# Optimization experiments

Measured on AMD Instinct MI355X. Metric: run time of the kernel, lower is better.

## Reference

```python
import jax, jax.numpy as jnp
import numpy as np

TAU = 0.001
TEMPERATURE = 0.1


def setup_inputs() -> dict:
    key = jax.random.key(0)
    k1, k2 = jax.random.split(key)
    B, H, N, L = 2, 8, 256, 64
    X = jax.random.normal(k1, (B, H, N, L), dtype=jnp.float32)
    Y = jax.random.normal(k2, (B, H, N, L), dtype=jnp.float32)
    return {"X": X, "Y": Y}


def _softsort_p2(scores):
    # scores: [B,H,N,L] -> s: [B,H,L,N]
    s = jnp.transpose(scores, (0, 1, 3, 2))
    srt = -jnp.sort(-s, axis=-1)  # descending sort along N
    # pairwise squared diff: rows = sorted values, cols = original values -> [B,H,L,N,N]
    pd = -((s[..., None, :] - srt[..., :, None]) ** 2) / TAU
    return jax.nn.softmax(pd, axis=-1)


def reference(X, Y):
    # Soft permutation matrices: [B,H,L,N,N]
    Pu = _softsort_p2(X)
    Pv = _softsort_p2(Y)
    # Gamma = Pu^T @ Pv  (contract over sorted-row index i)
    Gamma = jnp.einsum('bhlij,bhlik->bhljk', Pu, Pv)
    # cdist(X, Y, p=2) over last dim L -> [B,H,N,N]
    x2 = jnp.sum(X * X, axis=-1)            # [B,H,N]
    y2 = jnp.sum(Y * Y, axis=-1)            # [B,H,N]
    xy = jnp.einsum('bhnl,bhml->bhnm', X, Y)
    cost = jnp.sqrt(jnp.maximum(x2[..., :, None] + y2[..., None, :] - 2.0 * xy, 1e-12))
    # swds[b,h,l] = sum_{j,k} cost[b,h,j,k] * Gamma[b,h,l,j,k]
    swds = jnp.einsum('bhjk,bhljk->bhl', cost, Gamma)
    # exp(-T*(swds - min)) / sum == softmax(-T * swds) over L
    weights = jax.nn.softmax(-TEMPERATURE * swds, axis=-1)  # [B,H,L]
    # weighted sum over L -> [B,H,N,N]
    return jnp.einsum('bhljk,bhl->bhjk', Gamma, weights)
```

## Files before the change

### kernel.cpp

```cpp
#include <hip/hip_runtime.h>
#include <math.h>

#define INV_TAU 1000.0f
#define TEMP    0.1f
#define CEXP    -1442.6950408889634f


typedef __attribute__((ext_vector_type(8))) _Float16 half8;
typedef __attribute__((ext_vector_type(8))) short short8;
typedef __attribute__((ext_vector_type(4))) float f32x4;
typedef __attribute__((ext_vector_type(2))) unsigned int u32x2;

__device__ __forceinline__ float fexp2(float x) { return __builtin_amdgcn_exp2f(x); }

__device__ __forceinline__ half8 ldsh8(const unsigned short* p) {
  return __builtin_bit_cast(half8, *(const short8*)p);
}

__device__ __forceinline__ unsigned bf16r(float f) {
  unsigned u = __float_as_uint(f);
  return (u + 0x7FFFu + ((u >> 16) & 1u)) >> 16;
}

__device__ __forceinline__ int tswz(int row, int g) {
  return row * 32 + (((g + (row >> 1)) & 3) << 3);
}

__global__ __launch_bounds__(256) void prep_kernel(const float* __restrict__ X,
                                                   const float* __restrict__ Y,
                                                   float* __restrict__ cost,
                                                   float* __restrict__ srtu, float* __restrict__ lziu,
                                                   float* __restrict__ srtv, float* __restrict__ lziv) {
  __shared__ __align__(16) float smem[256];
  const int tid = threadIdx.x;
  if (blockIdx.x < 1024) {
    const int jq = blockIdx.x & 63, bh = blockIdx.x >> 6;
    const int j0 = jq * 4;
    smem[tid] = X[((size_t)bh*256 + j0 + (tid >> 6))*64 + (tid & 63)];
    __syncthreads();
    const float4* yp = (const float4*)(Y + ((size_t)bh*256 + tid)*64);
    float dot[4] = {0.f,0.f,0.f,0.f}, x2[4] = {0.f,0.f,0.f,0.f}, y2 = 0.f;
#pragma unroll
    for (int t = 0; t < 16; ++t) {
      float4 yv = yp[t];
      y2 += yv.x*yv.x + yv.y*yv.y + yv.z*yv.z + yv.w*yv.w;
#pragma unroll
      for (int r = 0; r < 4; ++r) {
        float4 xv = ((const float4*)(smem + r*64))[t];
        dot[r] += xv.x*yv.x + xv.y*yv.y + xv.z*yv.z + xv.w*yv.w;
        x2[r]  += xv.x*xv.x + xv.y*xv.y + xv.z*xv.z + xv.w*xv.w;
      }
    }
#pragma unroll
    for (int r = 0; r < 4; ++r) {
      float c = x2[r] + y2 - 2.f*dot[r];
      cost[((size_t)bh*256 + j0 + r)*256 + tid] = sqrtf(fmaxf(c, 1e-12f));
    }
  } else {
    const int idx = blockIdx.x - 1024;
    const int l = idx & 63, bh = (idx >> 6) & 15, uv = idx >> 10;
    const float* S = uv ? Y : X;
    float* so = uv ? srtv : srtu;
    float* zo = uv ? lziv : lziu;
    float v = S[((size_t)bh*256 + tid)*64 + l];
#pragma unroll
    for (int k = 2; k <= 256; k <<= 1) {
#pragma unroll
      for (int j = k >> 1; j > 0; j >>= 1) {
        float o;
        if (j >= 64) {
          smem[tid] = v; __syncthreads();
          o = smem[tid ^ j]; __syncthreads();
        } else {
          o = __shfl_xor(v, j, 64);
        }
        const bool up    = ((tid & k) == 0);
        const bool lower = ((tid & j) == 0);
        float mn = fminf(v, o), mx = fmaxf(v, o);
        v = (up == lower) ? mn : mx;
      }
    }
    smem[tid] = v; __syncthreads();
    const int jc = 255 - tid;
    const float sv = smem[jc];
    const int lo = jc > 48 ? jc - 48 : 0;
    const int hi = jc < 207 ? jc + 48 : 255;
    float z = 0.f;
    for (int jj = lo; jj <= hi; ++jj) { float d = smem[jj] - sv; z += fexp2(d*d*CEXP); }
    const int base = (bh*64 + l)*256 + tid;
    so[base] = sv; zo[base] = -__log2f(z);
  }
}

__device__ __forceinline__ void stage_slab(int t, int ib, float uval, float vval,
                                           const float* __restrict__ srtU, const float* __restrict__ lziU,
                                           const float* __restrict__ srtV, const float* __restrict__ lziV,
                                           unsigned short* __restrict__ EU,
                                           unsigned short* __restrict__ EV) {
  const int r  = t & 127;
  const int gp = (t >> 7) << 1;
  const int i0 = ib + (gp << 3);
#pragma unroll
  for (int gg = 0; gg < 2; ++gg) {
    float e[8];
#pragma unroll
    for (int ii = 0; ii < 8; ++ii) {
      float d = uval - srtU[i0 + gg*8 + ii];
      e[ii] = fexp2(fmaf(d*d, CEXP, lziU[i0 + gg*8 + ii]));
    }
    uint4 w;
    w.x = __builtin_bit_cast(unsigned, __builtin_amdgcn_cvt_pkrtz(e[0], e[1]));
    w.y = __builtin_bit_cast(unsigned, __builtin_amdgcn_cvt_pkrtz(e[2], e[3]));
    w.z = __builtin_bit_cast(unsigned, __builtin_amdgcn_cvt_pkrtz(e[4], e[5]));
    w.w = __builtin_bit_cast(unsigned, __builtin_amdgcn_cvt_pkrtz(e[6], e[7]));
    *(uint4*)&EU[tswz(r, gp + gg)] = w;
  }
#pragma unroll
  for (int gg = 0; gg < 2; ++gg) {
    float e[8];
#pragma unroll
    for (int ii = 0; ii < 8; ++ii) {
      float d = vval - srtV[i0 + gg*8 + ii];
      e[ii] = fexp2(fmaf(d*d, CEXP, lziV[i0 + gg*8 + ii]));
    }
    uint4 w;
    w.x = __builtin_bit_cast(unsigned, __builtin_amdgcn_cvt_pkrtz(e[0], e[1]));
    w.y = __builtin_bit_cast(unsigned, __builtin_amdgcn_cvt_pkrtz(e[2], e[3]));
    w.z = __builtin_bit_cast(unsigned, __builtin_amdgcn_cvt_pkrtz(e[4], e[5]));
    w.w = __builtin_bit_cast(unsigned, __builtin_amdgcn_cvt_pkrtz(e[6], e[7]));
    *(uint4*)&EV[tswz(r, gp + gg)] = w;
  }
}

__global__ __launch_bounds__(256, 4) void pass1_kernel(
    const float* __restrict__ X, const float* __restrict__ Y,
    const float* __restrict__ cost,
    const float* __restrict__ srtu, const float* __restrict__ lziu,
    const float* __restrict__ srtv, const float* __restrict__ lziv,
    float* __restrict__ parts, u32x2* __restrict__ gamma) {
  const int tile = blockIdx.x, l = blockIdx.y, bh = blockIdx.z;
  const int j0 = (tile >> 1) * 128, k0 = (tile & 1) * 128;
  const int tid = threadIdx.x, wave = tid >> 6, lane = tid & 63;
  const int wj = (wave & 1) * 64, wk = (wave >> 1) * 64;
  const int m = lane & 15, q = lane >> 4;
  const int inner = m*32 + (((q + (m >> 1)) & 3) << 3);

  __shared__ float srtU[256], lziU[256], srtV[256], lziV[256];
  __shared__ __align__(16) unsigned short EU0[128*32], EU1[128*32];
  __shared__ __align__(16) unsigned short EV0[128*32], EV1[128*32];
  __shared__ float red[4];

  const int lb = (bh*64 + l)*256;
  const int r  = tid & 127;
  const float uval = X[((size_t)bh*256 + j0 + r)*64 + l];
  const float vval = Y[((size_t)bh*256 + k0 + r)*64 + l];
  srtU[tid] = srtu[lb + tid]; lziU[tid] = lziu[lb + tid];
  srtV[tid] = srtv[lb + tid]; lziV[tid] = lziv[lb + tid];

  f32x4 acc[16];
#pragma unroll
  for (int t = 0; t < 16; ++t) acc[t] = (f32x4){0.f, 0.f, 0.f, 0.f};

  __syncthreads();
  stage_slab(tid, 0, uval, vval, srtU, lziU, srtV, lziV, EU0, EV0);
  __syncthreads();
#pragma unroll 1
  for (int s = 0; s < 8; ++s) {
    const unsigned short* EUc = (s & 1) ? EU1 : EU0;
    const unsigned short* EVc = (s & 1) ? EV1 : EV0;
    unsigned short* EUn = (s & 1) ? EU0 : EU1;
    unsigned short* EVn = (s & 1) ? EV0 : EV1;
    half8 A[4], B[4];
#pragma unroll
    for (int mt = 0; mt < 4; ++mt) A[mt] = ldsh8(&EUc[(wj + mt*16)*32 + inner]);
#pragma unroll
    for (int nt = 0; nt < 4; ++nt) B[nt] = ldsh8(&EVc[(wk + nt*16)*32 + inner]);
    if (s < 7)
      stage_slab(tid, (s+1)*32, uval, vval, srtU, lziU, srtV, lziV, EUn, EVn);
#pragma unroll
    for (int mt = 0; mt < 4; ++mt)
#pragma unroll
      for (int nt = 0; nt < 4; ++nt)
        acc[mt*4+nt] = __builtin_amdgcn_mfma_f32_16x16x32_f16(A[mt], B[nt], acc[mt*4+nt], 0, 0, 0);
    __syncthreads();
  }

  const float* cb = cost + (size_t)bh * 65536;
  const int gbase = ((bh*4 + tile)*4 + wave) * 16;
  float part = 0.f;
#pragma unroll
  for (int mt = 0; mt < 4; ++mt) {
#pragma unroll
    for (int nt = 0; nt < 4; ++nt) {
      const int col  = k0 + wk + nt*16 + m;
      const int rowb = j0 + wj + mt*16 + q*4;
      f32x4 a = acc[mt*4 + nt];
      part += a.x*cb[(size_t)(rowb+0)*256 + col] + a.y*cb[(size_t)(rowb+1)*256 + col]
            + a.z*cb[(size_t)(rowb+2)*256 + col] + a.w*cb[(size_t)(rowb+3)*256 + col];
      u32x2 pk;
      pk.x = bf16r(a.x) | (bf16r(a.y) << 16);
      pk.y = bf16r(a.z) | (bf16r(a.w) << 16);
      __builtin_nontemporal_store(pk, &gamma[((size_t)(gbase + mt*4 + nt)*64 + l)*64 + lane]);
    }
  }
#pragma unroll
  for (int o = 32; o > 0; o >>= 1) part += __shfl_down(part, o, 64);
  if (lane == 0) red[wave] = part;
  __syncthreads();
  if (tid == 0) parts[(size_t)tile*1024 + bh*64 + l] = red[0] + red[1] + red[2] + red[3];
}

__global__ __launch_bounds__(256) void wsum_kernel(const u32x2* __restrict__ g,
                                                   const float* __restrict__ parts,
                                                   float* __restrict__ out) {
  const int wv = threadIdx.x >> 6, lane = threadIdx.x & 63;
  const int bh = blockIdx.x >> 6;
  __shared__ float w[64];
  if (wv == 0) {
    float s = parts[bh*64 + lane] + parts[1024 + bh*64 + lane]
            + parts[2048 + bh*64 + lane] + parts[3072 + bh*64 + lane];
    float v = -TEMP * s * 1.4426950408889634f;
    float mx = v;
#pragma unroll
    for (int o = 32; o > 0; o >>= 1) mx = fmaxf(mx, __shfl_xor(mx, o, 64));
    float e = fexp2(v - mx);
    float ssum = e;
#pragma unroll
    for (int o = 32; o > 0; o >>= 1) ssum += __shfl_xor(ssum, o, 64);
    w[lane] = e / ssum;
  }
  __syncthreads();
  const int group = blockIdx.x * 4 + wv;
  const u32x2* gp = g + (size_t)group*4096 + lane;
  float4 acc = {0.f, 0.f, 0.f, 0.f};
#pragma unroll 8
  for (int l = 0; l < 64; ++l) {
    u32x2 pk = __builtin_nontemporal_load(gp + l*64);
    float wl = w[l];
    acc.x += wl * __uint_as_float(pk.x << 16);
    acc.y += wl * __uint_as_float(pk.x & 0xFFFF0000u);
    acc.z += wl * __uint_as_float(pk.y << 16);
    acc.w += wl * __uint_as_float(pk.y & 0xFFFF0000u);
  }
  const int frag = group & 15;
  const int idx  = group >> 4;
  const int wave = idx & 3, tile = (idx >> 2) & 3;
  const int mt = frag >> 2, nt = frag & 3;
  const int m = lane & 15, q = lane >> 4;
  const int row = (tile >> 1)*128 + (wave & 1)*64 + mt*16 + q*4;
  const int col = (tile & 1)*128 + (wave >> 1)*64 + nt*16 + m;
  float* ob = out + ((size_t)bh*256 + row)*256 + col;
  __builtin_nontemporal_store(acc.x, &ob[0]);
  __builtin_nontemporal_store(acc.y, &ob[256]);
  __builtin_nontemporal_store(acc.z, &ob[512]);
  __builtin_nontemporal_store(acc.w, &ob[768]);
}

extern "C" void kernel_launch(void* const* d_in, const int* in_sizes, int n_in,
                              void* d_out, int out_size, void* d_ws, size_t ws_size,
                              hipStream_t stream) {
  (void)in_sizes; (void)n_in; (void)out_size; (void)ws_size;
  const float* X = (const float*)d_in[0];
  const float* Y = (const float*)d_in[1];
  float* out = (float*)d_out;
  float* ws  = (float*)d_ws;
  float* cost  = ws;
  float* srtu  = ws   + 1048576;
  float* lziu  = srtu + 262144;
  float* srtv  = lziu + 262144;
  float* lziv  = srtv + 262144;
  float* parts = lziv + 262144;
  u32x2* gamma = (u32x2*)(parts + 4096);

  prep_kernel <<<dim3(3072),      256, 0, stream>>>(X, Y, cost, srtu, lziu, srtv, lziv);
  pass1_kernel<<<dim3(4, 64, 16), 256, 0, stream>>>(X, Y, cost, srtu, lziu, srtv, lziv,
                                                    parts, gamma);
  wsum_kernel <<<dim3(1024),      256, 0, stream>>>(gamma, parts, out);
}
```

Baseline: 169.5 us.

## Widen pass1 blocks to 128x256 tiles and prescale softsort exponent terms

Each pass1 block now has 8 waves and covers 128 rows by the full 256 columns, so the V-side exp tiles are computed once per row half instead of being recomputed for each of two column tiles. This cuts the total exp work for the soft permutation operands. The sorted values are prescaled by sqrt of the exponent constant in prep, so each element needs one add, one fma and an exp2, with no separate multiply. In exchange, LDS use per block roughly doubles and the grid is halved, which may reduce occupancy.

```diff
diff --git a/kernel.cpp b/kernel.cpp
--- a/kernel.cpp
+++ b/kernel.cpp
@@ -4,6 +4,7 @@
 #define INV_TAU 1000.0f
 #define TEMP    0.1f
 #define CEXP    -1442.6950408889634f
+#define SQRTC   37.98283767f
 
 
 typedef __attribute__((ext_vector_type(8))) _Float16 half8;
@@ -29,8 +30,8 @@
 __global__ __launch_bounds__(256) void prep_kernel(const float* __restrict__ X,
                                                    const float* __restrict__ Y,
                                                    float* __restrict__ cost,
-                                                   float* __restrict__ srtu, float* __restrict__ lziu,
-                                                   float* __restrict__ srtv, float* __restrict__ lziv) {
+                                                   float* __restrict__ nssu, float* __restrict__ lziu,
+                                                   float* __restrict__ nssv, float* __restrict__ lziv) {
   __shared__ __align__(16) float smem[256];
   const int tid = threadIdx.x;
   if (blockIdx.x < 1024) {
@@ -60,7 +61,7 @@
     const int idx = blockIdx.x - 1024;
     const int l = idx & 63, bh = (idx >> 6) & 15, uv = idx >> 10;
     const float* S = uv ? Y : X;
-    float* so = uv ? srtv : srtu;
+    float* so = uv ? nssv : nssu;
     float* zo = uv ? lziv : lziu;
     float v = S[((size_t)bh*256 + tid)*64 + l];
 #pragma unroll
@@ -88,81 +89,83 @@
     float z = 0.f;
     for (int jj = lo; jj <= hi; ++jj) { float d = smem[jj] - sv; z += fexp2(d*d*CEXP); }
     const int base = (bh*64 + l)*256 + tid;
-    so[base] = sv; zo[base] = -__log2f(z);
-  }
-}
-
-__device__ __forceinline__ void stage_slab(int t, int ib, float uval, float vval,
-                                           const float* __restrict__ srtU, const float* __restrict__ lziU,
-                                           const float* __restrict__ srtV, const float* __restrict__ lziV,
+    so[base] = -SQRTC * sv; zo[base] = -__log2f(z);
+  }
+}
+
+__device__ __forceinline__ void stage_slab(int t, int ib, float usc, float vsc,
+                                           const float* __restrict__ nssU, const float* __restrict__ lzU,
+                                           const float* __restrict__ nssV, const float* __restrict__ lzV,
                                            unsigned short* __restrict__ EU,
                                            unsigned short* __restrict__ EV) {
-  const int r  = t & 127;
-  const int gp = (t >> 7) << 1;
-  const int i0 = ib + (gp << 3);
-#pragma unroll
-  for (int gg = 0; gg < 2; ++gg) {
+  {
+    const int r = t & 127, g = t >> 7;
+    const int i0 = ib + (g << 3);
     float e[8];
 #pragma unroll
     for (int ii = 0; ii < 8; ++ii) {
-      float d = uval - srtU[i0 + gg*8 + ii];
-      e[ii] = fexp2(fmaf(d*d, CEXP, lziU[i0 + gg*8 + ii]));
+      float d = usc + nssU[i0 + ii];
+      e[ii] = fexp2(fmaf(-d, d, lzU[i0 + ii]));
     }
     uint4 w;
     w.x = __builtin_bit_cast(unsigned, __builtin_amdgcn_cvt_pkrtz(e[0], e[1]));
     w.y = __builtin_bit_cast(unsigned, __builtin_amdgcn_cvt_pkrtz(e[2], e[3]));
     w.z = __builtin_bit_cast(unsigned, __builtin_amdgcn_cvt_pkrtz(e[4], e[5]));
     w.w = __builtin_bit_cast(unsigned, __builtin_amdgcn_cvt_pkrtz(e[6], e[7]));
-    *(uint4*)&EU[tswz(r, gp + gg)] = w;
-  }
-#pragma unroll
-  for (int gg = 0; gg < 2; ++gg) {
-    float e[8];
-#pragma unroll
-    for (int ii = 0; ii < 8; ++ii) {
-      float d = vval - srtV[i0 + gg*8 + ii];
-      e[ii] = fexp2(fmaf(d*d, CEXP, lziV[i0 + gg*8 + ii]));
-    }
-    uint4 w;
-    w.x = __builtin_bit_cast(unsigned, __builtin_amdgcn_cvt_pkrtz(e[0], e[1]));
-    w.y = __builtin_bit_cast(unsigned, __builtin_amdgcn_cvt_pkrtz(e[2], e[3]));
-    w.z = __builtin_bit_cast(unsigned, __builtin_amdgcn_cvt_pkrtz(e[4], e[5]));
-    w.w = __builtin_bit_cast(unsigned, __builtin_amdgcn_cvt_pkrtz(e[6], e[7]));
-    *(uint4*)&EV[tswz(r, gp + gg)] = w;
-  }
-}
-
-__global__ __launch_bounds__(256, 4) void pass1_kernel(
+    *(uint4*)&EU[tswz(r, g)] = w;
+  }
+  {
+    const int r = t & 255;
+    const int gp = (t >> 8) << 1;
+#pragma unroll
+    for (int gg = 0; gg < 2; ++gg) {
+      const int i0 = ib + ((gp + gg) << 3);
+      float e[8];
+#pragma unroll
+      for (int ii = 0; ii < 8; ++ii) {
+        float d = vsc + nssV[i0 + ii];
+        e[ii] = fexp2(fmaf(-d, d, lzV[i0 + ii]));
+      }
+      uint4 w;
+      w.x = __builtin_bit_cast(unsigned, __builtin_amdgcn_cvt_pkrtz(e[0], e[1]));
+      w.y = __builtin_bit_cast(unsigned, __builtin_amdgcn_cvt_pkrtz(e[2], e[3]));
+      w.z = __builtin_bit_cast(unsigned, __builtin_amdgcn_cvt_pkrtz(e[4], e[5]));
+      w.w = __builtin_bit_cast(unsigned, __builtin_amdgcn_cvt_pkrtz(e[6], e[7]));
+      *(uint4*)&EV[tswz(r, gp + gg)] = w;
+    }
+  }
+}
+
+__global__ __launch_bounds__(512, 4) void pass1_kernel(
     const float* __restrict__ X, const float* __restrict__ Y,
     const float* __restrict__ cost,
-    const float* __restrict__ srtu, const float* __restrict__ lziu,
-    const float* __restrict__ srtv, const float* __restrict__ lziv,
+    const float* __restrict__ nssu, const float* __restrict__ lziu,
+    const float* __restrict__ nssv, const float* __restrict__ lziv,
     float* __restrict__ parts, u32x2* __restrict__ gamma) {
-  const int tile = blockIdx.x, l = blockIdx.y, bh = blockIdx.z;
-  const int j0 = (tile >> 1) * 128, k0 = (tile & 1) * 128;
+  const int sb = blockIdx.x, l = blockIdx.y, bh = blockIdx.z;
+  const int j0 = sb * 128;
   const int tid = threadIdx.x, wave = tid >> 6, lane = tid & 63;
   const int wj = (wave & 1) * 64, wk = (wave >> 1) * 64;
   const int m = lane & 15, q = lane >> 4;
   const int inner = m*32 + (((q + (m >> 1)) & 3) << 3);
 
-  __shared__ float srtU[256], lziU[256], srtV[256], lziV[256];
+  __shared__ float nssU[256], lzU[256], nssV[256], lzV[256];
   __shared__ __align__(16) unsigned short EU0[128*32], EU1[128*32];
-  __shared__ __align__(16) unsigned short EV0[128*32], EV1[128*32];
-  __shared__ float red[4];
+  __shared__ __align__(16) unsigned short EV0[256*32], EV1[256*32];
+  __shared__ float red[8];
 
   const int lb = (bh*64 + l)*256;
-  const int r  = tid & 127;
-  const float uval = X[((size_t)bh*256 + j0 + r)*64 + l];
-  const float vval = Y[((size_t)bh*256 + k0 + r)*64 + l];
-  srtU[tid] = srtu[lb + tid]; lziU[tid] = lziu[lb + tid];
-  srtV[tid] = srtv[lb + tid]; lziV[tid] = lziv[lb + tid];
+  const float usc = SQRTC * X[((size_t)bh*256 + j0 + (tid & 127))*64 + l];
+  const float vsc = SQRTC * Y[((size_t)bh*256 + (tid & 255))*64 + l];
+  if (tid < 256) { nssU[tid] = nssu[lb + tid]; lzU[tid] = lziu[lb + tid]; }
+  else { const int t2 = tid - 256; nssV[t2] = nssv[lb + t2]; lzV[t2] = lziv[lb + t2]; }
 
   f32x4 acc[16];
 #pragma unroll
   for (int t = 0; t < 16; ++t) acc[t] = (f32x4){0.f, 0.f, 0.f, 0.f};
 
   __syncthreads();
-  stage_slab(tid, 0, uval, vval, srtU, lziU, srtV, lziV, EU0, EV0);
+  stage_slab(tid, 0, usc, vsc, nssU, lzU, nssV, lzV, EU0, EV0);
   __syncthreads();
 #pragma unroll 1
   for (int s = 0; s < 8; ++s) {
@@ -176,7 +179,7 @@
 #pragma unroll
     for (int nt = 0; nt < 4; ++nt) B[nt] = ldsh8(&EVc[(wk + nt*16)*32 + inner]);
     if (s < 7)
-      stage_slab(tid, (s+1)*32, uval, vval, srtU, lziU, srtV, lziV, EUn, EVn);
+      stage_slab(tid, (s+1)*32, usc, vsc, nssU, lzU, nssV, lzV, EUn, EVn);
 #pragma unroll
     for (int mt = 0; mt < 4; ++mt)
 #pragma unroll
@@ -186,13 +189,13 @@
   }
 
   const float* cb = cost + (size_t)bh * 65536;
-  const int gbase = ((bh*4 + tile)*4 + wave) * 16;
+  const int gbase = ((bh*2 + sb)*8 + wave) * 16;
   float part = 0.f;
 #pragma unroll
   for (int mt = 0; mt < 4; ++mt) {
 #pragma unroll
     for (int nt = 0; nt < 4; ++nt) {
-      const int col  = k0 + wk + nt*16 + m;
+      const int col  = wk + nt*16 + m;
       const int rowb = j0 + wj + mt*16 + q*4;
       f32x4 a = acc[mt*4 + nt];
       part += a.x*cb[(size_t)(rowb+0)*256 + col] + a.y*cb[(size_t)(rowb+1)*256 + col]
@@ -207,7 +210,10 @@
   for (int o = 32; o > 0; o >>= 1) part += __shfl_down(part, o, 64);
   if (lane == 0) red[wave] = part;
   __syncthreads();
-  if (tid == 0) parts[(size_t)tile*1024 + bh*64 + l] = red[0] + red[1] + red[2] + red[3];
+  if (tid == 0) {
+    float s8 = red[0]+red[1]+red[2]+red[3]+red[4]+red[5]+red[6]+red[7];
+    parts[sb*1024 + bh*64 + l] = s8;
+  }
 }
 
 __global__ __launch_bounds__(256) void wsum_kernel(const u32x2* __restrict__ g,
@@ -217,8 +223,7 @@
   const int bh = blockIdx.x >> 6;
   __shared__ float w[64];
   if (wv == 0) {
-    float s = parts[bh*64 + lane] + parts[1024 + bh*64 + lane]
-            + parts[2048 + bh*64 + lane] + parts[3072 + bh*64 + lane];
+    float s = parts[bh*64 + lane] + parts[1024 + bh*64 + lane];
     float v = -TEMP * s * 1.4426950408889634f;
     float mx = v;
 #pragma unroll
@@ -244,11 +249,11 @@
   }
   const int frag = group & 15;
   const int idx  = group >> 4;
-  const int wave = idx & 3, tile = (idx >> 2) & 3;
+  const int wave = idx & 7, sbb = (idx >> 3) & 1;
   const int mt = frag >> 2, nt = frag & 3;
   const int m = lane & 15, q = lane >> 4;
-  const int row = (tile >> 1)*128 + (wave & 1)*64 + mt*16 + q*4;
-  const int col = (tile & 1)*128 + (wave >> 1)*64 + nt*16 + m;
+  const int row = sbb*128 + (wave & 1)*64 + mt*16 + q*4;
+  const int col = (wave >> 1)*64 + nt*16 + m;
   float* ob = out + ((size_t)bh*256 + row)*256 + col;
   __builtin_nontemporal_store(acc.x, &ob[0]);
   __builtin_nontemporal_store(acc.y, &ob[256]);
@@ -265,15 +270,15 @@
   float* out = (float*)d_out;
   float* ws  = (float*)d_ws;
   float* cost  = ws;
-  float* srtu  = ws   + 1048576;
-  float* lziu  = srtu + 262144;
-  float* srtv  = lziu + 262144;
-  float* lziv  = srtv + 262144;
+  float* nssu  = ws   + 1048576;
+  float* lziu  = nssu + 262144;
+  float* nssv  = lziu + 262144;
+  float* lziv  = nssv + 262144;
   float* parts = lziv + 262144;
-  u32x2* gamma = (u32x2*)(parts + 4096);
-
-  prep_kernel <<<dim3(3072),      256, 0, stream>>>(X, Y, cost, srtu, lziu, srtv, lziv);
-  pass1_kernel<<<dim3(4, 64, 16), 256, 0, stream>>>(X, Y, cost, srtu, lziu, srtv, lziv,
+  u32x2* gamma = (u32x2*)(parts + 2048);
+
+  prep_kernel <<<dim3(3072),      256, 0, stream>>>(X, Y, cost, nssu, lziu, nssv, lziv);
+  pass1_kernel<<<dim3(2, 64, 16), 512, 0, stream>>>(X, Y, cost, nssu, lziu, nssv, lziv,
                                                     parts, gamma);
   wsum_kernel <<<dim3(1024),      256, 0, stream>>>(gamma, parts, out);
 }
```

After: 162.8 us. -3.9%, faster.
